# Performance work log

Hardware: AMD Instinct MI355X
Metric: run time of the kernel (lower is better)

The kernel has to match this reference:

```python
import jax, jax.numpy as jnp
import numpy as np
import math

N_HEAD = 8
D_MODEL = 512
HEAD_SIZE = D_MODEL // N_HEAD
VOCAB = 16384
BLOCK = 512
LN_EPS = 1e-5


def sinusoidal_pe(max_len, dim):
    pos = np.arange(max_len)[:, None].astype(np.float32)
    div = np.exp(np.arange(0, dim, 2).astype(np.float32) * (-math.log(10000.0) / dim))
    pe = np.zeros((max_len, dim), dtype=np.float32)
    pe[:, 0::2] = np.sin(pos * div)
    pe[:, 1::2] = np.cos(pos * div)
    return jnp.asarray(pe)  # (max_len, hs)


def setup_inputs() -> dict:
    key = jax.random.key(0)
    ks = jax.random.split(key, 6)
    b, t = 4, BLOCK
    return {
        "x": jax.random.normal(ks[0], (b, t, 1), dtype=jnp.float32),
        "embedding": jax.random.normal(ks[1], (N_HEAD, VOCAB, HEAD_SIZE), dtype=jnp.float32),
        "enc_w": jax.random.normal(ks[2], (D_MODEL, 1), dtype=jnp.float32) * 0.05,
        "enc_b": jax.random.normal(ks[3], (D_MODEL,), dtype=jnp.float32) * 0.05,
        "ln_w": jnp.ones((HEAD_SIZE,), dtype=jnp.float32),
        "ln_b": jnp.zeros((HEAD_SIZE,), dtype=jnp.float32),
        "dec_w": jax.random.normal(ks[4], (1, D_MODEL), dtype=jnp.float32) * 0.05,
        "dec_b": jax.random.normal(ks[5], (1,), dtype=jnp.float32) * 0.05,
    }


def reference(x, embedding, enc_w, enc_b, ln_w, ln_b, dec_w, dec_b):
    b, t, _ = x.shape
    # encoder: Linear(input_dim -> d_model)
    h = x @ enc_w.T + enc_b                              # (b, t, d_model)
    h = h.reshape(b, t, N_HEAD, HEAD_SIZE).transpose(0, 2, 1, 3)  # (b, nh, t, hs)
    # sinusoidal positional encoding over time, added to head dim
    h = h + sinusoidal_pe(BLOCK, HEAD_SIZE)[:t]
    # LayerNorm over hs
    mu = h.mean(-1, keepdims=True)
    var = ((h - mu) ** 2).mean(-1, keepdims=True)
    h = (h - mu) * jax.lax.rsqrt(var + LN_EPS) * ln_w + ln_b
    # attention over shared per-head codebook
    scores = jnp.einsum('bnth,nvh->bntv', h, embedding) / math.sqrt(D_MODEL)
    probs = jax.nn.softmax(scores, axis=-1)              # (b, nh, t, vocab)
    quant = jnp.einsum('bntv,nvh->bnth', probs, embedding)
    quant = quant.transpose(0, 2, 1, 3).reshape(b, t, D_MODEL)
    # decoder: Linear(d_model -> output_dim)
    return quant @ dec_w.T + dec_b                       # (b, t, 1)
```

## Files before the change

kernel.cpp:

```cpp
#include <hip/hip_runtime.h>
#include <hip/hip_bf16.h>
#include <math.h>

#define NH 8
#define HS 64
#define VOCAB 16384
#define QPH 2048
#define NVG 8
#define QSCALE (0.04419417382415922f * 1.4426950408889634f)

typedef __attribute__((ext_vector_type(8))) short bf16x8;
typedef __attribute__((ext_vector_type(4))) float f32x4;

static __device__ __forceinline__ unsigned short f2bf(float f) {
    __hip_bfloat16 h = __float2bfloat16(f);
    unsigned short u;
    __builtin_memcpy(&u, &h, 2);
    return u;
}

static __device__ __forceinline__ float fexp2(float x) {
#if __has_builtin(__builtin_amdgcn_exp2f)
    return __builtin_amdgcn_exp2f(x);
#else
    return __expf(x * 0.6931471805599453f);
#endif
}

static __device__ __forceinline__ void stage16(const void* g, void* l) {
    __builtin_amdgcn_global_load_lds(
        (const __attribute__((address_space(1))) void*)g,
        (__attribute__((address_space(3))) void*)l, 16, 0, 0);
}

__global__ void eprep(const float* __restrict__ emb, const float* __restrict__ dec_w,
                      unsigned short* __restrict__ ebf, float* __restrict__ g) {
    __shared__ ushort4 lu[256];
    __shared__ float red[16];
    int tid = threadIdx.x;
    int nt  = blockIdx.x;
    int n   = nt >> 10;
    int r   = tid >> 4;
    int c4  = tid & 15;
    f32x4 vv = ((const f32x4*)emb)[(size_t)nt * 256 + tid];
    ushort4 u = make_ushort4(f2bf(vv.x), f2bf(vv.y), f2bf(vv.z), f2bf(vv.w));
    int h = c4 >> 3, q = (c4 >> 1) & 3, jh = c4 & 1;
    lu[h * 128 + q * 32 + r * 2 + jh] = u;
    const float* dw = dec_w + n * 64 + c4 * 4;
    float p = vv.x * dw[0] + vv.y * dw[1] + vv.z * dw[2] + vv.w * dw[3];
    p += __shfl_xor(p, 1); p += __shfl_xor(p, 2);
    p += __shfl_xor(p, 4); p += __shfl_xor(p, 8);
    if (c4 == 0) red[r] = p;
    __syncthreads();
    ((ushort4*)ebf)[(size_t)nt * 256 + tid] = lu[tid];
    if (tid < 16) g[n * VOCAB + (nt & 1023) * 16 + tid] = red[tid];
}

__global__ void qprep(const float* __restrict__ x, const float* __restrict__ enc_w,
                      const float* __restrict__ enc_b, const float* __restrict__ ln_w,
                      const float* __restrict__ ln_b, unsigned short* __restrict__ qbf) {
    int h = threadIdx.x;
    int t = blockIdx.x;
    float h2  = (float)(h & ~1);
    float div = __expf(h2 * (-9.210340371976184f / 64.0f));
    float ang = (float)t * div;
    float pe  = (h & 1) ? __cosf(ang) : __sinf(ang);
    float lw = ln_w[h], lb = ln_b[h];
    int kf = h >> 5, quad = (h >> 3) & 3, j = h & 7;
    int fragoff = ((kf * 4 + quad) * 128) + j;
    #pragma unroll
    for (int n = 0; n < NH; ++n) {
        float ew = enc_w[n * 64 + h];
        float eb = enc_b[n * 64 + h];
        #pragma unroll
        for (int b = 0; b < 4; ++b) {
            int q = b * 512 + t;
            float v = x[q] * ew + eb + pe;
            float s = v;
            #pragma unroll
            for (int off = 1; off < 64; off <<= 1) s += __shfl_xor(s, off);
            float mu = s * (1.0f / 64.0f);
            float dd = v - mu;
            float s2 = dd * dd;
            #pragma unroll
            for (int off = 1; off < 64; off <<= 1) s2 += __shfl_xor(s2, off);
            float var = s2 * (1.0f / 64.0f);
            float y = dd * rsqrtf(var + 1e-5f) * lw + lb;
            int qt = (q >> 4) & 3, l15 = q & 15;
            size_t idx = ((size_t)(n * 32 + (q >> 6)) * 4096)
                       + qt * 1024 + l15 * 8 + fragoff;
            qbf[idx] = f2bf(y * QSCALE);
        }
    }
}

__global__ void __launch_bounds__(256, 2)
attn(const unsigned short* __restrict__ qbf, const unsigned short* __restrict__ ebf,
     const float* __restrict__ g, float2* __restrict__ part) {
    __shared__ __attribute__((aligned(16))) char smem[73728];
    int tid  = threadIdx.x;
    int w    = tid >> 6;
    int lane = tid & 63;
    int quad = lane >> 4;
    int l15  = lane & 15;
    int head   = blockIdx.x & 7;
    int vgroup = (blockIdx.x >> 3) & 7;
    int qchunk = blockIdx.x >> 6;

    char*  eb = smem + w * 8192;
    char*  qw = smem + 32768 + w * 8192;
    float* gl = (float*)(smem + 65536);

    const char* qsrc = (const char*)qbf + (size_t)(head * 32 + qchunk * 4 + w) * 8192;
    const char* esrc = (const char*)ebf + (size_t)head * 2097152 + (size_t)vgroup * 262144;
    const char* gsrc = (const char*)(g + head * VOCAB + vgroup * 2048);

    #pragma unroll
    for (int c = 0; c < 8; ++c)
        stage16(qsrc + c * 1024 + lane * 16, qw + c * 1024);
    stage16(gsrc + (w * 2)     * 1024 + lane * 16, (char*)gl + (w * 2)     * 1024);
    stage16(gsrc + (w * 2 + 1) * 1024 + lane * 16, (char*)gl + (w * 2 + 1) * 1024);
    #pragma unroll
    for (int c = 0; c < 4; ++c)
        stage16(esrc + c * 1024 + lane * 16, eb + c * 1024);
    __syncthreads();

    float num[4] = {0.f, 0.f, 0.f, 0.f};
    float den[4] = {0.f, 0.f, 0.f, 0.f};
    const f32x4 z = {0.f, 0.f, 0.f, 0.f};
    const char*  el   = eb + lane * 16;
    const char*  qr   = qw + lane * 16;
    const float* glq  = gl + quad * 4;
    const char*  srcp = esrc + 4096 + lane * 16;

    #pragma clang loop unroll(disable)
    for (int t = 0; t < 64; ++t) {
        char* pd = eb + ((t + 1) & 1) * 4096;
        stage16(srcp,        pd);
        stage16(srcp + 1024, pd + 1024);
        stage16(srcp + 2048, pd + 2048);
        stage16(srcp + 3072, pd + 3072);
        srcp += 4096;
        asm volatile("s_waitcnt vmcnt(4)" ::: "memory");
        __builtin_amdgcn_sched_barrier(0);

        const char* ebb = el + (t & 1) * 4096;
        bf16x8 a00 = *(const bf16x8*)(ebb);
        bf16x8 a01 = *(const bf16x8*)(ebb + 1024);
        bf16x8 a10 = *(const bf16x8*)(ebb + 2048);
        bf16x8 a11 = *(const bf16x8*)(ebb + 3072);
        f32x4 gv0 = *(const f32x4*)(glq + t * 32);
        f32x4 gv1 = *(const f32x4*)(glq + t * 32 + 16);

        #pragma unroll
        for (int qt = 0; qt < 4; ++qt) {
            bf16x8 q0 = *(const bf16x8*)(qr + qt * 2048);
            bf16x8 q1 = *(const bf16x8*)(qr + qt * 2048 + 1024);
            f32x4 acc0 = __builtin_amdgcn_mfma_f32_16x16x32_bf16(a00, q0, z, 0, 0, 0);
            acc0       = __builtin_amdgcn_mfma_f32_16x16x32_bf16(a01, q1, acc0, 0, 0, 0);
            f32x4 acc1 = __builtin_amdgcn_mfma_f32_16x16x32_bf16(a10, q0, z, 0, 0, 0);
            acc1       = __builtin_amdgcn_mfma_f32_16x16x32_bf16(a11, q1, acc1, 0, 0, 0);
            #pragma unroll
            for (int r = 0; r < 4; ++r) {
                float p0 = fexp2(acc0[r]);
                float p1 = fexp2(acc1[r]);
                den[qt] += p0 + p1;
                num[qt] += p0 * gv0[r] + p1 * gv1[r];
            }
        }
    }

    #pragma unroll
    for (int qt = 0; qt < 4; ++qt) {
        num[qt] += __shfl_xor(num[qt], 16); num[qt] += __shfl_xor(num[qt], 32);
        den[qt] += __shfl_xor(den[qt], 16); den[qt] += __shfl_xor(den[qt], 32);
    }
    float nv = quad == 0 ? num[0] : quad == 1 ? num[1] : quad == 2 ? num[2] : num[3];
    float dv = quad == 0 ? den[0] : quad == 1 ? den[1] : quad == 2 ? den[2] : den[3];
    int qg = qchunk * 256 + w * 64 + quad * 16 + l15;
    part[((size_t)vgroup * NH + head) * QPH + qg] = make_float2(nv, dv);
}

__global__ void fin(const float2* __restrict__ part, const float* __restrict__ dec_b,
                    float* __restrict__ out) {
    __shared__ float red[8][32];
    int t  = threadIdx.x;
    int ql = t & 31;
    int n  = t >> 5;
    int q  = blockIdx.x * 32 + ql;
    float nv = 0.f, dv = 0.f;
    #pragma unroll
    for (int sl = 0; sl < NVG; ++sl) {
        float2 nd = part[((size_t)sl * NH + n) * QPH + q];
        nv += nd.x; dv += nd.y;
    }
    red[n][ql] = nv / dv;
    __syncthreads();
    if (t < 32) {
        float s = dec_b[0];
        #pragma unroll
        for (int m = 0; m < NH; ++m) s += red[m][t];
        out[q] = s;
    }
}

extern "C" void kernel_launch(void* const* d_in, const int* in_sizes, int n_in,
                              void* d_out, int out_size, void* d_ws, size_t ws_size,
                              hipStream_t stream) {
    const float* x     = (const float*)d_in[0];
    const float* emb   = (const float*)d_in[1];
    const float* enc_w = (const float*)d_in[2];
    const float* enc_b = (const float*)d_in[3];
    const float* ln_w  = (const float*)d_in[4];
    const float* ln_b  = (const float*)d_in[5];
    const float* dec_w = (const float*)d_in[6];
    const float* dec_b = (const float*)d_in[7];
    float* out = (float*)d_out;

    char* ws = (char*)d_ws;
    unsigned short* qbf  = (unsigned short*)(ws);
    unsigned short* ebf  = (unsigned short*)(ws + 2097152);
    float*          g    = (float*)(ws + 2097152 + 16777216);
    float2*         part = (float2*)(ws + 2097152 + 16777216 + 524288);

    hipLaunchKernelGGL(eprep, dim3(8192), dim3(256), 0, stream, emb, dec_w, ebf, g);
    hipLaunchKernelGGL(qprep, dim3(512),  dim3(64),  0, stream, x, enc_w, enc_b, ln_w, ln_b, qbf);
    hipLaunchKernelGGL(attn,  dim3(512),  dim3(256), 0, stream, qbf, ebf, g, part);
    hipLaunchKernelGGL(fin,   dim3(64),   dim3(256), 0, stream, part, dec_b, out);
}
```

Before: 160.4 us.

## Merge prep kernels into one launch and hold Q fragments in registers

Merges the embedding conversion and query LayerNorm prep kernels into a single launch, with the extra blocks handling four timesteps each. This removes one kernel launch and the serialization between the two prep kernels. The attention kernel now loads its Q fragments straight from global memory into registers instead of staging them through LDS. That shrinks LDS from 72KB to 40KB per block and drops the per-iteration LDS reads of Q, at the cost of more VGPRs under the 2-blocks-per-SM launch bound.

```diff
diff --git a/kernel.cpp b/kernel.cpp
--- a/kernel.cpp
+++ b/kernel.cpp
@@ -33,63 +33,65 @@
         (__attribute__((address_space(3))) void*)l, 16, 0, 0);
 }
 
-__global__ void eprep(const float* __restrict__ emb, const float* __restrict__ dec_w,
-                      unsigned short* __restrict__ ebf, float* __restrict__ g) {
+__global__ void prep(const float* __restrict__ emb, const float* __restrict__ dec_w,
+                     const float* __restrict__ x, const float* __restrict__ enc_w,
+                     const float* __restrict__ enc_b, const float* __restrict__ ln_w,
+                     const float* __restrict__ ln_b,
+                     unsigned short* __restrict__ ebf, float* __restrict__ g,
+                     unsigned short* __restrict__ qbf) {
     __shared__ ushort4 lu[256];
     __shared__ float red[16];
     int tid = threadIdx.x;
-    int nt  = blockIdx.x;
-    int n   = nt >> 10;
-    int r   = tid >> 4;
-    int c4  = tid & 15;
-    f32x4 vv = ((const f32x4*)emb)[(size_t)nt * 256 + tid];
-    ushort4 u = make_ushort4(f2bf(vv.x), f2bf(vv.y), f2bf(vv.z), f2bf(vv.w));
-    int h = c4 >> 3, q = (c4 >> 1) & 3, jh = c4 & 1;
-    lu[h * 128 + q * 32 + r * 2 + jh] = u;
-    const float* dw = dec_w + n * 64 + c4 * 4;
-    float p = vv.x * dw[0] + vv.y * dw[1] + vv.z * dw[2] + vv.w * dw[3];
-    p += __shfl_xor(p, 1); p += __shfl_xor(p, 2);
-    p += __shfl_xor(p, 4); p += __shfl_xor(p, 8);
-    if (c4 == 0) red[r] = p;
-    __syncthreads();
-    ((ushort4*)ebf)[(size_t)nt * 256 + tid] = lu[tid];
-    if (tid < 16) g[n * VOCAB + (nt & 1023) * 16 + tid] = red[tid];
-}
-
-__global__ void qprep(const float* __restrict__ x, const float* __restrict__ enc_w,
-                      const float* __restrict__ enc_b, const float* __restrict__ ln_w,
-                      const float* __restrict__ ln_b, unsigned short* __restrict__ qbf) {
-    int h = threadIdx.x;
-    int t = blockIdx.x;
-    float h2  = (float)(h & ~1);
-    float div = __expf(h2 * (-9.210340371976184f / 64.0f));
-    float ang = (float)t * div;
-    float pe  = (h & 1) ? __cosf(ang) : __sinf(ang);
-    float lw = ln_w[h], lb = ln_b[h];
-    int kf = h >> 5, quad = (h >> 3) & 3, j = h & 7;
-    int fragoff = ((kf * 4 + quad) * 128) + j;
-    #pragma unroll
-    for (int n = 0; n < NH; ++n) {
-        float ew = enc_w[n * 64 + h];
-        float eb = enc_b[n * 64 + h];
+    if (blockIdx.x < 8192) {
+        int nt  = blockIdx.x;
+        int n   = nt >> 10;
+        int r   = tid >> 4;
+        int c4  = tid & 15;
+        f32x4 vv = ((const f32x4*)emb)[(size_t)nt * 256 + tid];
+        ushort4 u = make_ushort4(f2bf(vv.x), f2bf(vv.y), f2bf(vv.z), f2bf(vv.w));
+        int h = c4 >> 3, q = (c4 >> 1) & 3, jh = c4 & 1;
+        lu[h * 128 + q * 32 + r * 2 + jh] = u;
+        const float* dw = dec_w + n * 64 + c4 * 4;
+        float p = vv.x * dw[0] + vv.y * dw[1] + vv.z * dw[2] + vv.w * dw[3];
+        p += __shfl_xor(p, 1); p += __shfl_xor(p, 2);
+        p += __shfl_xor(p, 4); p += __shfl_xor(p, 8);
+        if (c4 == 0) red[r] = p;
+        __syncthreads();
+        ((ushort4*)ebf)[(size_t)nt * 256 + tid] = lu[tid];
+        if (tid < 16) g[n * VOCAB + (nt & 1023) * 16 + tid] = red[tid];
+    } else {
+        int h = tid & 63;
+        int t = (blockIdx.x - 8192) * 4 + (tid >> 6);
+        float h2  = (float)(h & ~1);
+        float div = __expf(h2 * (-9.210340371976184f / 64.0f));
+        float ang = (float)t * div;
+        float pe  = (h & 1) ? __cosf(ang) : __sinf(ang);
+        float lw = ln_w[h], lb = ln_b[h];
+        int kf = h >> 5, quad = (h >> 3) & 3, j = h & 7;
+        int fragoff = ((kf * 4 + quad) * 128) + j;
         #pragma unroll
-        for (int b = 0; b < 4; ++b) {
-            int q = b * 512 + t;
-            float v = x[q] * ew + eb + pe;
-            float s = v;
+        for (int n = 0; n < NH; ++n) {
+            float ew = enc_w[n * 64 + h];
+            float eb = enc_b[n * 64 + h];
             #pragma unroll
-            for (int off = 1; off < 64; off <<= 1) s += __shfl_xor(s, off);
-            float mu = s * (1.0f / 64.0f);
-            float dd = v - mu;
-            float s2 = dd * dd;
-            #pragma unroll
-            for (int off = 1; off < 64; off <<= 1) s2 += __shfl_xor(s2, off);
-            float var = s2 * (1.0f / 64.0f);
-            float y = dd * rsqrtf(var + 1e-5f) * lw + lb;
-            int qt = (q >> 4) & 3, l15 = q & 15;
-            size_t idx = ((size_t)(n * 32 + (q >> 6)) * 4096)
-                       + qt * 1024 + l15 * 8 + fragoff;
-            qbf[idx] = f2bf(y * QSCALE);
+            for (int b = 0; b < 4; ++b) {
+                int q = b * 512 + t;
+                float v = x[q] * ew + eb + pe;
+                float s = v;
+                #pragma unroll
+                for (int off = 1; off < 64; off <<= 1) s += __shfl_xor(s, off);
+                float mu = s * (1.0f / 64.0f);
+                float dd = v - mu;
+                float s2 = dd * dd;
+                #pragma unroll
+                for (int off = 1; off < 64; off <<= 1) s2 += __shfl_xor(s2, off);
+                float var = s2 * (1.0f / 64.0f);
+                float y = dd * rsqrtf(var + 1e-5f) * lw + lb;
+                int qt = (q >> 4) & 3, l15 = q & 15;
+                size_t idx = ((size_t)(n * 32 + (q >> 6)) * 4096)
+                           + qt * 1024 + l15 * 8 + fragoff;
+                qbf[idx] = f2bf(y * QSCALE);
+            }
         }
     }
 }
@@ -97,7 +99,7 @@
 __global__ void __launch_bounds__(256, 2)
 attn(const unsigned short* __restrict__ qbf, const unsigned short* __restrict__ ebf,
      const float* __restrict__ g, float2* __restrict__ part) {
-    __shared__ __attribute__((aligned(16))) char smem[73728];
+    __shared__ __attribute__((aligned(16))) char smem[32768 + 8192];
     int tid  = threadIdx.x;
     int w    = tid >> 6;
     int lane = tid & 63;
@@ -108,28 +110,30 @@
     int qchunk = blockIdx.x >> 6;
 
     char*  eb = smem + w * 8192;
-    char*  qw = smem + 32768 + w * 8192;
-    float* gl = (float*)(smem + 65536);
+    float* gl = (float*)(smem + 32768);
 
     const char* qsrc = (const char*)qbf + (size_t)(head * 32 + qchunk * 4 + w) * 8192;
     const char* esrc = (const char*)ebf + (size_t)head * 2097152 + (size_t)vgroup * 262144;
     const char* gsrc = (const char*)(g + head * VOCAB + vgroup * 2048);
 
-    #pragma unroll
-    for (int c = 0; c < 8; ++c)
-        stage16(qsrc + c * 1024 + lane * 16, qw + c * 1024);
     stage16(gsrc + (w * 2)     * 1024 + lane * 16, (char*)gl + (w * 2)     * 1024);
     stage16(gsrc + (w * 2 + 1) * 1024 + lane * 16, (char*)gl + (w * 2 + 1) * 1024);
     #pragma unroll
     for (int c = 0; c < 4; ++c)
         stage16(esrc + c * 1024 + lane * 16, eb + c * 1024);
     __syncthreads();
+
+    bf16x8 qf0[4], qf1[4];
+    #pragma unroll
+    for (int qt = 0; qt < 4; ++qt) {
+        qf0[qt] = *(const bf16x8*)(qsrc + (qt * 2)     * 1024 + lane * 16);
+        qf1[qt] = *(const bf16x8*)(qsrc + (qt * 2 + 1) * 1024 + lane * 16);
+    }
 
     float num[4] = {0.f, 0.f, 0.f, 0.f};
     float den[4] = {0.f, 0.f, 0.f, 0.f};
     const f32x4 z = {0.f, 0.f, 0.f, 0.f};
     const char*  el   = eb + lane * 16;
-    const char*  qr   = qw + lane * 16;
     const float* glq  = gl + quad * 4;
     const char*  srcp = esrc + 4096 + lane * 16;
 
@@ -154,12 +158,10 @@
 
         #pragma unroll
         for (int qt = 0; qt < 4; ++qt) {
-            bf16x8 q0 = *(const bf16x8*)(qr + qt * 2048);
-            bf16x8 q1 = *(const bf16x8*)(qr + qt * 2048 + 1024);
-            f32x4 acc0 = __builtin_amdgcn_mfma_f32_16x16x32_bf16(a00, q0, z, 0, 0, 0);
-            acc0       = __builtin_amdgcn_mfma_f32_16x16x32_bf16(a01, q1, acc0, 0, 0, 0);
-            f32x4 acc1 = __builtin_amdgcn_mfma_f32_16x16x32_bf16(a10, q0, z, 0, 0, 0);
-            acc1       = __builtin_amdgcn_mfma_f32_16x16x32_bf16(a11, q1, acc1, 0, 0, 0);
+            f32x4 acc0 = __builtin_amdgcn_mfma_f32_16x16x32_bf16(a00, qf0[qt], z, 0, 0, 0);
+            acc0       = __builtin_amdgcn_mfma_f32_16x16x32_bf16(a01, qf1[qt], acc0, 0, 0, 0);
+            f32x4 acc1 = __builtin_amdgcn_mfma_f32_16x16x32_bf16(a10, qf0[qt], z, 0, 0, 0);
+            acc1       = __builtin_amdgcn_mfma_f32_16x16x32_bf16(a11, qf1[qt], acc1, 0, 0, 0);
             #pragma unroll
             for (int r = 0; r < 4; ++r) {
                 float p0 = fexp2(acc0[r]);
@@ -223,8 +225,8 @@
     float*          g    = (float*)(ws + 2097152 + 16777216);
     float2*         part = (float2*)(ws + 2097152 + 16777216 + 524288);
 
-    hipLaunchKernelGGL(eprep, dim3(8192), dim3(256), 0, stream, emb, dec_w, ebf, g);
-    hipLaunchKernelGGL(qprep, dim3(512),  dim3(64),  0, stream, x, enc_w, enc_b, ln_w, ln_b, qbf);
-    hipLaunchKernelGGL(attn,  dim3(512),  dim3(256), 0, stream, qbf, ebf, g, part);
-    hipLaunchKernelGGL(fin,   dim3(64),   dim3(256), 0, stream, part, dec_b, out);
-}
+    hipLaunchKernelGGL(prep, dim3(8320), dim3(256), 0, stream,
+                       emb, dec_w, x, enc_w, enc_b, ln_w, ln_b, ebf, g, qbf);
+    hipLaunchKernelGGL(attn, dim3(512),  dim3(256), 0, stream, qbf, ebf, g, part);
+    hipLaunchKernelGGL(fin,  dim3(64),   dim3(256), 0, stream, part, dec_b, out);
+}
```

Result: no change. 159.0 us (-0.9%).
